# Kernel tuning notes

Hardware: AMD Instinct MI355X
Metric: run time of the kernel (lower is better)

Reference implementation:

```python
import jax, jax.numpy as jnp
import numpy as np

B, S, D = 1024, 48, 256   # graphs, nodes-per-graph, embedding dim (= input_dim)
GDIM = 512                # graph_dim
N = B * S                 # total nodes
E = 4 * N                 # directed edges (avg degree ~4, molecular graphs)
W_SCALE = 0.05


def setup_inputs() -> dict:
    key = jax.random.key(0)
    ks = jax.random.split(key, 8)
    return {
        "sub2gene_out": jax.random.normal(ks[0], (B, S, D), jnp.float32),
        "edge_index": jax.random.randint(ks[1], (2, E), 0, N, dtype=jnp.int64),
        # conv1: in_channels = 2*D (concat of x and laplacian-smoothed x)
        "W_l1": jax.random.normal(ks[2], (GDIM, 2 * D), jnp.float32) * W_SCALE,
        "W_r1": jax.random.normal(ks[3], (GDIM, 2 * D), jnp.float32) * W_SCALE,
        "b1": jnp.zeros((GDIM,), jnp.float32),
        # conv2: graph_dim -> graph_dim
        "W_l2": jax.random.normal(ks[4], (GDIM, GDIM), jnp.float32) * W_SCALE,
        "W_r2": jax.random.normal(ks[5], (GDIM, GDIM), jnp.float32) * W_SCALE,
        "b2": jnp.zeros((GDIM,), jnp.float32),
    }


def sage_conv(x, src, dst, W_l, W_r, b, n):
    """PyG SAGEConv (mean aggregation, root_weight=True):
    out_i = W_l @ mean_{j in N(i)} x_j + W_r @ x_i + b, messages flow src->dst."""
    msg = x[src]                                            # [E, F] gather
    agg = jax.ops.segment_sum(msg, dst, num_segments=n)     # [N, F]
    cnt = jax.ops.segment_sum(jnp.ones((src.shape[0],), x.dtype), dst, num_segments=n)
    mean = agg / jnp.maximum(cnt, 1.0)[:, None]
    return mean @ W_l.T + x @ W_r.T + b


def reference(sub2gene_out, edge_index, W_l1, W_r1, b1, W_l2, W_r2, b2):
    b_, s_, d_ = sub2gene_out.shape
    n = b_ * s_
    x = sub2gene_out.reshape(n, d_)                         # cat of per-graph node features
    row, col = edge_index[0], edge_index[1]

    # sym-normalized Laplacian L = I - D^{-1/2} A D^{-1/2}; lap_x = L @ x
    ones_e = jnp.ones((row.shape[0],), x.dtype)
    deg = jax.ops.segment_sum(ones_e, row, num_segments=n)
    dinv = jnp.where(deg > 0, 1.0, 0.0) / jnp.sqrt(jnp.maximum(deg, 1.0))
    w = -(dinv[row] * dinv[col])                            # off-diagonal -A_norm
    lap_x = x + jax.ops.segment_sum(w[:, None] * x[col], row, num_segments=n)

    x_comb = jnp.concatenate([x, lap_x], axis=-1)           # [N, 2D]
    h = jax.nn.gelu(sage_conv(x_comb, row, col, W_l1, W_r1, b1, n), approximate=False)
    h = sage_conv(h, row, col, W_l2, W_r2, b2, n)           # [N, GDIM]

    # global_mean_pool: every graph has exactly s_ nodes
    batch = jnp.repeat(jnp.arange(b_), s_)
    pooled = jax.ops.segment_sum(h, batch, num_segments=b_) / jnp.asarray(s_, h.dtype)
    return pooled                                           # [B, GDIM]
```

## Files before the change

kernel.cpp:

```cpp
#include <hip/hip_runtime.h>
#include <math.h>

typedef unsigned short u16;
typedef __attribute__((ext_vector_type(8))) short bf16x8;
typedef __attribute__((ext_vector_type(4))) float f32x4;

#define NB 1024
#define NS 48
#define ND 256
#define NN (NB*NS)
#define NE (4*NN)
#define GD 512

__device__ __forceinline__ void gld16(const void* g, void* l) {
  __builtin_amdgcn_global_load_lds(
      (const __attribute__((address_space(1))) void*)(void*)g,
      (__attribute__((address_space(3))) void*)l, 16, 0, 0);
}

__device__ __forceinline__ float bf2f(u16 h) {
  unsigned u = ((unsigned)h) << 16; float f; __builtin_memcpy(&f, &u, 4); return f;
}
__device__ __forceinline__ u16 f2bf(float f) {
  unsigned u; __builtin_memcpy(&u, &f, 4);
  u += 0x7fffu + ((u >> 16) & 1u);
  return (u16)(u >> 16);
}
__device__ __forceinline__ void unpack4(uint2 v, float* f) {
  f[0]=bf2f((u16)(v.x & 0xffff)); f[1]=bf2f((u16)(v.x >> 16));
  f[2]=bf2f((u16)(v.y & 0xffff)); f[3]=bf2f((u16)(v.y >> 16));
}
__device__ __forceinline__ void unpack8(uint4 v, float* f) {
  f[0]=bf2f((u16)(v.x & 0xffff)); f[1]=bf2f((u16)(v.x >> 16));
  f[2]=bf2f((u16)(v.y & 0xffff)); f[3]=bf2f((u16)(v.y >> 16));
  f[4]=bf2f((u16)(v.z & 0xffff)); f[5]=bf2f((u16)(v.z >> 16));
  f[6]=bf2f((u16)(v.w & 0xffff)); f[7]=bf2f((u16)(v.w >> 16));
}
__device__ __forceinline__ uint4 pack8(const float* f) {
  uint4 v;
  v.x = (unsigned)f2bf(f[0]) | ((unsigned)f2bf(f[1]) << 16);
  v.y = (unsigned)f2bf(f[2]) | ((unsigned)f2bf(f[3]) << 16);
  v.z = (unsigned)f2bf(f[4]) | ((unsigned)f2bf(f[5]) << 16);
  v.w = (unsigned)f2bf(f[6]) | ((unsigned)f2bf(f[7]) << 16);
  return v;
}


__global__ void k_hist(const int* __restrict__ ei, int* __restrict__ deg, int* __restrict__ cnt) {
  int e = blockIdx.x * 256 + threadIdx.x;
  if (e < NE) {
    atomicAdd(&deg[ei[e]], 1);
    atomicAdd(&cnt[ei[NE + e]], 1);
  }
}

__global__ void k_dinv(const int* __restrict__ deg, float* __restrict__ dinv) {
  int i = blockIdx.x * 256 + threadIdx.x;
  if (i < NN) dinv[i] = (deg[i] > 0) ? rsqrtf((float)deg[i]) : 0.0f;
}

__global__ void k_exscan(const int* __restrict__ in, int* __restrict__ out) {
  __shared__ int sums[1024];
  const int t = threadIdx.x;
  const int base = t * 48;
  int s = 0;
  for (int i = 0; i < 48; ++i) s += in[base + i];
  sums[t] = s;
  __syncthreads();
  for (int off = 1; off < 1024; off <<= 1) {
    int v = (t >= off) ? sums[t - off] : 0;
    __syncthreads();
    sums[t] += v;
    __syncthreads();
  }
  int run = (t == 0) ? 0 : sums[t - 1];
  for (int i = 0; i < 48; ++i) { int v = in[base + i]; out[base + i] = run; run += v; }
  if (t == 1023) out[NN] = run;
}

__global__ void k_fill(const int* __restrict__ ei,
                       const int* __restrict__ rowOff, const int* __restrict__ colOff,
                       int* __restrict__ rowFill, int* __restrict__ colFill,
                       int* __restrict__ rowCol, int* __restrict__ colSrc) {
  int e = blockIdx.x * 256 + threadIdx.x;
  if (e < NE) {
    int r = ei[e], c = ei[NE + e];
    int pr = atomicAdd(&rowFill[r], 1);
    rowCol[rowOff[r] + pr] = c;
    int pc = atomicAdd(&colFill[c], 1);
    colSrc[colOff[c] + pc] = r;
  }
}

__global__ void k_wcat(const float* __restrict__ W, u16* __restrict__ Wc) {
  int i = (blockIdx.x * 256 + threadIdx.x) * 4;
  float4 v = *(const float4*)(W + i);
  ushort4 h; h.x = f2bf(v.x); h.y = f2bf(v.y); h.z = f2bf(v.z); h.w = f2bf(v.w);
  *(ushort4*)(Wc + i) = h;
}

__global__ void k_x2bf(const float* __restrict__ x, u16* __restrict__ xb) {
  int i = (blockIdx.x * 256 + threadIdx.x) * 8;
  float4 v0 = *(const float4*)(x + i);
  float4 v1 = *(const float4*)(x + i + 4);
  float f[8] = {v0.x, v0.y, v0.z, v0.w, v1.x, v1.y, v1.z, v1.w};
  *(uint4*)(xb + i) = pack8(f);
}

__global__ void k_lap(const u16* __restrict__ xb, const int* __restrict__ rowOff,
                      const int* __restrict__ rowCol, const float* __restrict__ dinv,
                      u16* __restrict__ xc) {
  const int gid = blockIdx.x * 256 + threadIdx.x;
  const int node = gid >> 6, lane = gid & 63;
  float xi[4]; unpack4(*(const uint2*)(xb + (size_t)node * ND + lane * 4), xi);
  float a0 = 0.f, a1 = 0.f, a2 = 0.f, a3 = 0.f;
  const int s0 = rowOff[node], s1 = rowOff[node + 1];
  for (int p = s0; p < s1; p += 4) {
    const int q1 = (p + 1 < s1) ? p + 1 : s1 - 1;
    const int q2 = (p + 2 < s1) ? p + 2 : s1 - 1;
    const int q3 = (p + 3 < s1) ? p + 3 : s1 - 1;
    const int c0 = rowCol[p], c1 = rowCol[q1], c2 = rowCol[q2], c3 = rowCol[q3];
    const float w0 = dinv[c0];
    const float w1 = (p + 1 < s1) ? dinv[c1] : 0.f;
    const float w2 = (p + 2 < s1) ? dinv[c2] : 0.f;
    const float w3 = (p + 3 < s1) ? dinv[c3] : 0.f;
    float f0[4], f1[4], f2[4], f3[4];
    unpack4(*(const uint2*)(xb + (size_t)c0 * ND + lane * 4), f0);
    unpack4(*(const uint2*)(xb + (size_t)c1 * ND + lane * 4), f1);
    unpack4(*(const uint2*)(xb + (size_t)c2 * ND + lane * 4), f2);
    unpack4(*(const uint2*)(xb + (size_t)c3 * ND + lane * 4), f3);
    a0 += w0 * f0[0] + w1 * f1[0] + w2 * f2[0] + w3 * f3[0];
    a1 += w0 * f0[1] + w1 * f1[1] + w2 * f2[1] + w3 * f3[1];
    a2 += w0 * f0[2] + w1 * f1[2] + w2 * f2[2] + w3 * f3[2];
    a3 += w0 * f0[3] + w1 * f1[3] + w2 * f2[3] + w3 * f3[3];
  }
  const float di = dinv[node];
  u16* dst = xc + (size_t)node * GD + lane * 4;
  ushort4 hx; hx.x = f2bf(xi[0]); hx.y = f2bf(xi[1]); hx.z = f2bf(xi[2]); hx.w = f2bf(xi[3]);
  *(ushort4*)dst = hx;
  ushort4 hl; hl.x = f2bf(xi[0] - di * a0); hl.y = f2bf(xi[1] - di * a1);
  hl.z = f2bf(xi[2] - di * a2); hl.w = f2bf(xi[3] - di * a3);
  *(ushort4*)(dst + ND) = hl;
}

__global__ void k_aggx(const u16* __restrict__ xc, const int* __restrict__ colOff,
                       const int* __restrict__ colSrc, u16* __restrict__ xagg) {
  const int gid = blockIdx.x * 256 + threadIdx.x;
  const int node = gid >> 6, lane = gid & 63;
  const int f0 = lane * 8;
  float acc[8] = {};
  const int s0 = colOff[node], s1 = colOff[node + 1];
  for (int p = s0; p < s1; p += 4) {
    const int q1 = (p + 1 < s1) ? p + 1 : s1 - 1;
    const int q2 = (p + 2 < s1) ? p + 2 : s1 - 1;
    const int q3 = (p + 3 < s1) ? p + 3 : s1 - 1;
    const int c0 = colSrc[p], c1 = colSrc[q1], c2 = colSrc[q2], c3 = colSrc[q3];
    const float w1 = (p + 1 < s1) ? 1.f : 0.f;
    const float w2 = (p + 2 < s1) ? 1.f : 0.f;
    const float w3 = (p + 3 < s1) ? 1.f : 0.f;
    float g0[8], g1[8], g2[8], g3[8];
    unpack8(*(const uint4*)(xc + (size_t)c0 * GD + f0), g0);
    unpack8(*(const uint4*)(xc + (size_t)c1 * GD + f0), g1);
    unpack8(*(const uint4*)(xc + (size_t)c2 * GD + f0), g2);
    unpack8(*(const uint4*)(xc + (size_t)c3 * GD + f0), g3);
    #pragma unroll
    for (int j = 0; j < 8; ++j) acc[j] += g0[j] + w1 * g1[j] + w2 * g2[j] + w3 * g3[j];
  }
  const float inv = (s1 > s0) ? 1.0f / (float)(s1 - s0) : 1.0f;
  float res[8];
  #pragma unroll
  for (int j = 0; j < 8; ++j) res[j] = acc[j] * inv;
  *(uint4*)(xagg + (size_t)node * GD + f0) = pack8(res);
}

template <int MODE>
__global__ __launch_bounds__(256) void k_gemm(const u16* __restrict__ A0,
                                              const u16* __restrict__ A1,
                                              const u16* __restrict__ B0,
                                              const u16* __restrict__ B1,
                                              const float* __restrict__ bias,
                                              void* __restrict__ OutP) {
  __shared__ u16 As[128 * 32];
  __shared__ u16 Bs[128 * 32];
  const int tid = threadIdx.x;
  const int w = tid >> 6, lane = tid & 63;
  const int wr = w >> 1, wc = w & 1;

  const int cpx = gridDim.x >> 3;
  const int o = blockIdx.x;
  const int swz = (o & 7) * cpx + (o >> 3);
  const int bx = swz >> 2;
  const int by = swz & 3;

  const int c0 = w * 2, c1 = c0 + 1;
  const int lrow = lane >> 2;
  const int lcol = ((lane & 3) ^ ((lane >> 3) & 3)) * 8;
  const size_t a0r = (size_t)(bx * 128 + c0 * 16 + lrow) * GD + lcol;
  const size_t a1r = (size_t)(bx * 128 + c1 * 16 + lrow) * GD + lcol;
  const size_t b0r = (size_t)(by * 128 + c0 * 16 + lrow) * GD + lcol;
  const size_t b1r = (size_t)(by * 128 + c1 * 16 + lrow) * GD + lcol;
  u16* As0 = As + c0 * 512; u16* As1 = As + c1 * 512;
  u16* Bs0 = Bs + c0 * 512; u16* Bs1 = Bs + c1 * 512;

  const int kslot = ((lane >> 4) ^ ((lane >> 1) & 3)) * 8;
  const int aoff = (wr * 64 + (lane & 15)) * 32 + kslot;
  const int boff = (wc * 64 + (lane & 15)) * 32 + kslot;

  f32x4 acc[4][4] = {};

  for (int kt = 0; kt < 1024; kt += 32) {
    const u16* Asrc = (kt < 512) ? A0 + kt : A1 + (kt - 512);
    const u16* Bsrc = (kt < 512) ? B0 + kt : B1 + (kt - 512);
    gld16(Asrc + a0r, As0);
    gld16(Asrc + a1r, As1);
    gld16(Bsrc + b0r, Bs0);
    gld16(Bsrc + b1r, Bs1);
    __syncthreads();
    bf16x8 aF[4], bF[4];
    #pragma unroll
    for (int i = 0; i < 4; ++i) aF[i] = *(const bf16x8*)(As + aoff + i * 512);
    #pragma unroll
    for (int i = 0; i < 4; ++i) bF[i] = *(const bf16x8*)(Bs + boff + i * 512);
    #pragma unroll
    for (int mi = 0; mi < 4; ++mi)
      #pragma unroll
      for (int ni = 0; ni < 4; ++ni)
        acc[mi][ni] = __builtin_amdgcn_mfma_f32_16x16x32_bf16(aF[mi], bF[ni], acc[mi][ni], 0, 0, 0);
    __syncthreads();
  }

  const int lc = lane & 15, lr = (lane >> 4) * 4;
  const size_t r0 = (size_t)bx * 128 + wr * 64;
  const int cb = by * 128 + wc * 64;
  float bv[4];
  #pragma unroll
  for (int ni = 0; ni < 4; ++ni) bv[ni] = bias[cb + ni * 16 + lc];
  #pragma unroll
  for (int mi = 0; mi < 4; ++mi)
    #pragma unroll
    for (int ni = 0; ni < 4; ++ni)
      #pragma unroll
      for (int r = 0; r < 4; ++r) {
        float v = acc[mi][ni][r] + bv[ni];
        const size_t idx = (r0 + mi * 16 + lr + r) * GD + (cb + ni * 16 + lc);
        if (MODE == 0) {
          v = 0.5f * v * (1.0f + erff(v * 0.70710678118654752f));
          ((u16*)OutP)[idx] = f2bf(v);
        } else {
          ((float*)OutP)[idx] = v;
        }
      }
}

__global__ __launch_bounds__(256) void k_aggh(const u16* __restrict__ h, const int* __restrict__ colOff,
                                              const int* __restrict__ colSrc,
                                              u16* __restrict__ hrb, u16* __restrict__ hab) {
  __shared__ float red[2][4][GD];
  const int g = blockIdx.x;
  const int t = threadIdx.x, w = t >> 6, lane = t & 63;
  const int f0 = lane * 8;
  float pr[8] = {}, pa[8] = {};
  for (int n = w; n < NS; n += 4) {
    const int node = g * NS + n;
    float tmp[8];
    unpack8(*(const uint4*)(h + (size_t)node * GD + f0), tmp);
    #pragma unroll
    for (int j = 0; j < 8; ++j) pr[j] += tmp[j];
    float acc[8] = {};
    const int s0 = colOff[node], s1 = colOff[node + 1];
    for (int p = s0; p < s1; p += 4) {
      const int q1 = (p + 1 < s1) ? p + 1 : s1 - 1;
      const int q2 = (p + 2 < s1) ? p + 2 : s1 - 1;
      const int q3 = (p + 3 < s1) ? p + 3 : s1 - 1;
      const int c0 = colSrc[p], c1 = colSrc[q1], c2 = colSrc[q2], c3 = colSrc[q3];
      const float w1 = (p + 1 < s1) ? 1.f : 0.f;
      const float w2 = (p + 2 < s1) ? 1.f : 0.f;
      const float w3 = (p + 3 < s1) ? 1.f : 0.f;
      float g0[8], g1[8], g2[8], g3[8];
      unpack8(*(const uint4*)(h + (size_t)c0 * GD + f0), g0);
      unpack8(*(const uint4*)(h + (size_t)c1 * GD + f0), g1);
      unpack8(*(const uint4*)(h + (size_t)c2 * GD + f0), g2);
      unpack8(*(const uint4*)(h + (size_t)c3 * GD + f0), g3);
      #pragma unroll
      for (int j = 0; j < 8; ++j) acc[j] += g0[j] + w1 * g1[j] + w2 * g2[j] + w3 * g3[j];
    }
    const float inv = (s1 > s0) ? 1.0f / (float)(s1 - s0) : 1.0f;
    #pragma unroll
    for (int j = 0; j < 8; ++j) pa[j] += acc[j] * inv;
  }
  #pragma unroll
  for (int j = 0; j < 8; ++j) { red[0][w][f0 + j] = pr[j]; red[1][w][f0 + j] = pa[j]; }
  __syncthreads();
  const int f = t * 2;
  const float invS = 1.0f / (float)NS;
  float r0 = (red[0][0][f] + red[0][1][f] + red[0][2][f] + red[0][3][f]) * invS;
  float r1 = (red[0][0][f+1] + red[0][1][f+1] + red[0][2][f+1] + red[0][3][f+1]) * invS;
  float a0 = (red[1][0][f] + red[1][1][f] + red[1][2][f] + red[1][3][f]) * invS;
  float a1 = (red[1][0][f+1] + red[1][1][f+1] + red[1][2][f+1] + red[1][3][f+1]) * invS;
  *(unsigned*)(hrb + (size_t)g * GD + f) = (unsigned)f2bf(r0) | ((unsigned)f2bf(r1) << 16);
  *(unsigned*)(hab + (size_t)g * GD + f) = (unsigned)f2bf(a0) | ((unsigned)f2bf(a1) << 16);
}

extern "C" void kernel_launch(void* const* d_in, const int* in_sizes, int n_in,
                              void* d_out, int out_size, void* d_ws, size_t ws_size,
                              hipStream_t stream) {
  const float* x   = (const float*)d_in[0];
  const int*   ei  = (const int*)d_in[1];
  const float* Wl1 = (const float*)d_in[2];
  const float* Wr1 = (const float*)d_in[3];
  const float* b1  = (const float*)d_in[4];
  const float* Wl2 = (const float*)d_in[5];
  const float* Wr2 = (const float*)d_in[6];
  const float* b2  = (const float*)d_in[7];
  float* out = (float*)d_out;
  (void)in_sizes; (void)n_in; (void)out_size; (void)ws_size;

  int* deg     = (int*)d_ws;
  int* cnt     = deg + NN;
  int* rowFill = cnt + NN;
  int* colFill = rowFill + NN;
  int* rowOff  = colFill + NN;
  int* colOff  = rowOff + NN + 64;
  float* dinv  = (float*)(colOff + NN + 64);
  int* rowCol  = (int*)(dinv + NN);
  int* colSrc  = rowCol + NE;
  u16* WcR1    = (u16*)(colSrc + NE);
  u16* WcL1    = WcR1 + 512 * 512;
  u16* WcR2    = WcL1 + 512 * 512;
  u16* WcL2    = WcR2 + 512 * 512;
  u16* xc      = WcL2 + 512 * 512;
  u16* xagg    = xc + (size_t)NN * GD;
  u16* h       = xagg + (size_t)NN * GD;
  u16* xb      = h;
  u16* hrb     = xagg;
  u16* hab     = xagg + 1024 * GD;

  hipMemsetAsync(deg, 0, sizeof(int) * 4 * NN, stream);

  k_hist<<<NE / 256, 256, 0, stream>>>(ei, deg, cnt);
  k_dinv<<<NN / 256, 256, 0, stream>>>(deg, dinv);
  k_exscan<<<1, 1024, 0, stream>>>(deg, rowOff);
  k_exscan<<<1, 1024, 0, stream>>>(cnt, colOff);
  k_fill<<<NE / 256, 256, 0, stream>>>(ei, rowOff, colOff, rowFill, colFill, rowCol, colSrc);
  k_wcat<<<256, 256, 0, stream>>>(Wr1, WcR1);
  k_wcat<<<256, 256, 0, stream>>>(Wl1, WcL1);
  k_wcat<<<256, 256, 0, stream>>>(Wr2, WcR2);
  k_wcat<<<256, 256, 0, stream>>>(Wl2, WcL2);
  k_x2bf<<<(NN * ND) / (256 * 8), 256, 0, stream>>>(x, xb);
  k_lap<<<(NN * 64) / 256, 256, 0, stream>>>(xb, rowOff, rowCol, dinv, xc);
  k_aggx<<<(NN * 64) / 256, 256, 0, stream>>>(xc, colOff, colSrc, xagg);

  k_gemm<0><<<(NN / 128) * 4, 256, 0, stream>>>(xc, xagg, WcR1, WcL1, b1, (void*)h);

  k_aggh<<<NB, 256, 0, stream>>>(h, colOff, colSrc, hrb, hab);

  k_gemm<1><<<(NB / 128) * 4, 256, 0, stream>>>(hrb, hab, WcR2, WcL2, b2, (void*)out);
}
```

Measured before the change: 295.1 us.

## Double-buffer GEMM LDS tiles and merge scan and weight-convert launches

The bf16 MFMA GEMM now uses two LDS buffers, issuing the next k-tile's global-to-LDS loads before computing the current one, with an explicit vmcnt wait and raw barriers in place of the load-sync-compute-sync loop. The two exclusive-scan launches are merged into one two-block launch, and the four weight-conversion launches into one. The aim is to hide global load latency inside the GEMM and cut kernel launch overhead, at the cost of doubled LDS use per block, which may lower occupancy.

After: 281.3 us. 4.7% less time.

```diff
diff --git a/kernel.cpp b/kernel.cpp
--- a/kernel.cpp
+++ b/kernel.cpp
@@ -59,8 +59,11 @@
   if (i < NN) dinv[i] = (deg[i] > 0) ? rsqrtf((float)deg[i]) : 0.0f;
 }
 
-__global__ void k_exscan(const int* __restrict__ in, int* __restrict__ out) {
+__global__ void k_exscan2(const int* __restrict__ deg, const int* __restrict__ cnt,
+                          int* __restrict__ rowOff, int* __restrict__ colOff) {
   __shared__ int sums[1024];
+  const int* in = blockIdx.x ? cnt : deg;
+  int* out = blockIdx.x ? colOff : rowOff;
   const int t = threadIdx.x;
   const int base = t * 48;
   int s = 0;
@@ -92,9 +95,14 @@
   }
 }
 
-__global__ void k_wcat(const float* __restrict__ W, u16* __restrict__ Wc) {
+__global__ void k_wall(const float* __restrict__ Wr1, const float* __restrict__ Wl1,
+                       const float* __restrict__ Wr2, const float* __restrict__ Wl2,
+                       u16* __restrict__ Wc) {
   int i = (blockIdx.x * 256 + threadIdx.x) * 4;
-  float4 v = *(const float4*)(W + i);
+  int which = i >> 18;
+  int off = i & 262143;
+  const float* W = (which == 0) ? Wr1 : (which == 1) ? Wl1 : (which == 2) ? Wr2 : Wl2;
+  float4 v = *(const float4*)(W + off);
   ushort4 h; h.x = f2bf(v.x); h.y = f2bf(v.y); h.z = f2bf(v.z); h.w = f2bf(v.w);
   *(ushort4*)(Wc + i) = h;
 }
@@ -180,8 +188,8 @@
                                               const u16* __restrict__ B1,
                                               const float* __restrict__ bias,
                                               void* __restrict__ OutP) {
-  __shared__ u16 As[128 * 32];
-  __shared__ u16 Bs[128 * 32];
+  __shared__ u16 As[2][128 * 32];
+  __shared__ u16 Bs[2][128 * 32];
   const int tid = threadIdx.x;
   const int w = tid >> 6, lane = tid & 63;
   const int wr = w >> 1, wc = w & 1;
@@ -199,8 +207,6 @@
   const size_t a1r = (size_t)(bx * 128 + c1 * 16 + lrow) * GD + lcol;
   const size_t b0r = (size_t)(by * 128 + c0 * 16 + lrow) * GD + lcol;
   const size_t b1r = (size_t)(by * 128 + c1 * 16 + lrow) * GD + lcol;
-  u16* As0 = As + c0 * 512; u16* As1 = As + c1 * 512;
-  u16* Bs0 = Bs + c0 * 512; u16* Bs1 = Bs + c1 * 512;
 
   const int kslot = ((lane >> 4) ^ ((lane >> 1) & 3)) * 8;
   const int aoff = (wr * 64 + (lane & 15)) * 32 + kslot;
@@ -208,26 +214,43 @@
 
   f32x4 acc[4][4] = {};
 
-  for (int kt = 0; kt < 1024; kt += 32) {
-    const u16* Asrc = (kt < 512) ? A0 + kt : A1 + (kt - 512);
-    const u16* Bsrc = (kt < 512) ? B0 + kt : B1 + (kt - 512);
-    gld16(Asrc + a0r, As0);
-    gld16(Asrc + a1r, As1);
-    gld16(Bsrc + b0r, Bs0);
-    gld16(Bsrc + b1r, Bs1);
-    __syncthreads();
-    bf16x8 aF[4], bF[4];
-    #pragma unroll
-    for (int i = 0; i < 4; ++i) aF[i] = *(const bf16x8*)(As + aoff + i * 512);
-    #pragma unroll
-    for (int i = 0; i < 4; ++i) bF[i] = *(const bf16x8*)(Bs + boff + i * 512);
-    #pragma unroll
-    for (int mi = 0; mi < 4; ++mi)
-      #pragma unroll
-      for (int ni = 0; ni < 4; ++ni)
-        acc[mi][ni] = __builtin_amdgcn_mfma_f32_16x16x32_bf16(aF[mi], bF[ni], acc[mi][ni], 0, 0, 0);
-    __syncthreads();
-  }
+  #define STAGE(kt, buf) do {                                              \
+    const u16* Asrc_ = ((kt) < 512) ? A0 + (kt) : A1 + ((kt) - 512);       \
+    const u16* Bsrc_ = ((kt) < 512) ? B0 + (kt) : B1 + ((kt) - 512);       \
+    gld16(Asrc_ + a0r, As[buf] + c0 * 512);                                \
+    gld16(Asrc_ + a1r, As[buf] + c1 * 512);                                \
+    gld16(Bsrc_ + b0r, Bs[buf] + c0 * 512);                                \
+    gld16(Bsrc_ + b1r, Bs[buf] + c1 * 512);                                \
+  } while (0)
+
+  #define COMPUTE(buf) do {                                                \
+    bf16x8 aF[4], bF[4];                                                   \
+    _Pragma("unroll")                                                      \
+    for (int i = 0; i < 4; ++i) aF[i] = *(const bf16x8*)(As[buf] + aoff + i * 512); \
+    _Pragma("unroll")                                                      \
+    for (int i = 0; i < 4; ++i) bF[i] = *(const bf16x8*)(Bs[buf] + boff + i * 512); \
+    _Pragma("unroll")                                                      \
+    for (int mi = 0; mi < 4; ++mi)                                         \
+      _Pragma("unroll")                                                    \
+      for (int ni = 0; ni < 4; ++ni)                                       \
+        acc[mi][ni] = __builtin_amdgcn_mfma_f32_16x16x32_bf16(aF[mi], bF[ni], acc[mi][ni], 0, 0, 0); \
+  } while (0)
+
+  STAGE(0, 0);
+  int cur = 0;
+  for (int t = 0; t < 31; ++t) {
+    STAGE((t + 1) * 32, cur ^ 1);
+    asm volatile("s_waitcnt vmcnt(4)" ::: "memory");
+    __builtin_amdgcn_s_barrier();
+    COMPUTE(cur);
+    __builtin_amdgcn_s_barrier();
+    cur ^= 1;
+  }
+  asm volatile("s_waitcnt vmcnt(0)" ::: "memory");
+  __builtin_amdgcn_s_barrier();
+  COMPUTE(cur);
+  #undef STAGE
+  #undef COMPUTE
 
   const int lc = lane & 15, lr = (lane >> 4) * 4;
   const size_t r0 = (size_t)bx * 128 + wr * 64;
@@ -339,13 +362,9 @@
 
   k_hist<<<NE / 256, 256, 0, stream>>>(ei, deg, cnt);
   k_dinv<<<NN / 256, 256, 0, stream>>>(deg, dinv);
-  k_exscan<<<1, 1024, 0, stream>>>(deg, rowOff);
-  k_exscan<<<1, 1024, 0, stream>>>(cnt, colOff);
+  k_exscan2<<<2, 1024, 0, stream>>>(deg, cnt, rowOff, colOff);
   k_fill<<<NE / 256, 256, 0, stream>>>(ei, rowOff, colOff, rowFill, colFill, rowCol, colSrc);
-  k_wcat<<<256, 256, 0, stream>>>(Wr1, WcR1);
-  k_wcat<<<256, 256, 0, stream>>>(Wl1, WcL1);
-  k_wcat<<<256, 256, 0, stream>>>(Wr2, WcR2);
-  k_wcat<<<256, 256, 0, stream>>>(Wl2, WcL2);
+  k_wall<<<1024, 256, 0, stream>>>(Wr1, Wl1, Wr2, Wl2, WcR1);
   k_x2bf<<<(NN * ND) / (256 * 8), 256, 0, stream>>>(x, xb);
   k_lap<<<(NN * 64) / 256, 256, 0, stream>>>(xb, rowOff, rowCol, dinv, xc);
   k_aggx<<<(NN * 64) / 256, 256, 0, stream>>>(xc, colOff, colSrc, xagg);
```

## Merge small setup kernels, widen Laplacian gather, split GEMM K loop

Applied to the files above, without the earlier changes.

Folds the dinv computation and both exclusive scans into one three-block launch. Merges the four weight conversions and the x-to-bf16 conversion into one kernel. The Laplacian kernel now handles two nodes per wavefront with 8-element (16-byte) loads, halving its grid. The GEMM K loop is split into two unrolled halves so the per-iteration source-pointer selects go away. Together these cut launch count and per-thread overhead, at the cost of a few branches inside the fused kernels.

New measurement: 288.2 us. 1.02x faster.

```diff
diff --git a/kernel.cpp b/kernel.cpp
--- a/kernel.cpp
+++ b/kernel.cpp
@@ -25,10 +25,6 @@
   unsigned u; __builtin_memcpy(&u, &f, 4);
   u += 0x7fffu + ((u >> 16) & 1u);
   return (u16)(u >> 16);
-}
-__device__ __forceinline__ void unpack4(uint2 v, float* f) {
-  f[0]=bf2f((u16)(v.x & 0xffff)); f[1]=bf2f((u16)(v.x >> 16));
-  f[2]=bf2f((u16)(v.y & 0xffff)); f[3]=bf2f((u16)(v.y >> 16));
 }
 __device__ __forceinline__ void unpack8(uint4 v, float* f) {
   f[0]=bf2f((u16)(v.x & 0xffff)); f[1]=bf2f((u16)(v.x >> 16));
@@ -54,15 +50,21 @@
   }
 }
 
-__global__ void k_dinv(const int* __restrict__ deg, float* __restrict__ dinv) {
-  int i = blockIdx.x * 256 + threadIdx.x;
-  if (i < NN) dinv[i] = (deg[i] > 0) ? rsqrtf((float)deg[i]) : 0.0f;
-}
-
-__global__ void k_exscan(const int* __restrict__ in, int* __restrict__ out) {
-  __shared__ int sums[1024];
+__global__ void k_exscan2(const int* __restrict__ deg, const int* __restrict__ cnt,
+                          int* __restrict__ rowOff, int* __restrict__ colOff,
+                          float* __restrict__ dinv) {
   const int t = threadIdx.x;
   const int base = t * 48;
+  if (blockIdx.x == 2) {
+    for (int i = 0; i < 48; ++i) {
+      int d = deg[base + i];
+      dinv[base + i] = (d > 0) ? rsqrtf((float)d) : 0.0f;
+    }
+    return;
+  }
+  __shared__ int sums[1024];
+  const int* in = blockIdx.x ? cnt : deg;
+  int* out = blockIdx.x ? colOff : rowOff;
   int s = 0;
   for (int i = 0; i < 48; ++i) s += in[base + i];
   sums[t] = s;
@@ -92,28 +94,35 @@
   }
 }
 
-__global__ void k_wcat(const float* __restrict__ W, u16* __restrict__ Wc) {
-  int i = (blockIdx.x * 256 + threadIdx.x) * 4;
-  float4 v = *(const float4*)(W + i);
-  ushort4 h; h.x = f2bf(v.x); h.y = f2bf(v.y); h.z = f2bf(v.z); h.w = f2bf(v.w);
-  *(ushort4*)(Wc + i) = h;
-}
-
-__global__ void k_x2bf(const float* __restrict__ x, u16* __restrict__ xb) {
-  int i = (blockIdx.x * 256 + threadIdx.x) * 8;
-  float4 v0 = *(const float4*)(x + i);
-  float4 v1 = *(const float4*)(x + i + 4);
-  float f[8] = {v0.x, v0.y, v0.z, v0.w, v1.x, v1.y, v1.z, v1.w};
-  *(uint4*)(xb + i) = pack8(f);
+__global__ void k_wx(const float* __restrict__ Wr1, const float* __restrict__ Wl1,
+                     const float* __restrict__ Wr2, const float* __restrict__ Wl2,
+                     u16* __restrict__ Wc, const float* __restrict__ x, u16* __restrict__ xb) {
+  if (blockIdx.x < 1024) {
+    int i = (blockIdx.x * 256 + threadIdx.x) * 4;
+    int which = i >> 18;
+    int off = i & 262143;
+    const float* W = (which == 0) ? Wr1 : (which == 1) ? Wl1 : (which == 2) ? Wr2 : Wl2;
+    float4 v = *(const float4*)(W + off);
+    ushort4 h; h.x = f2bf(v.x); h.y = f2bf(v.y); h.z = f2bf(v.z); h.w = f2bf(v.w);
+    *(ushort4*)(Wc + i) = h;
+  } else {
+    int i = ((blockIdx.x - 1024) * 256 + threadIdx.x) * 8;
+    float4 v0 = *(const float4*)(x + i);
+    float4 v1 = *(const float4*)(x + i + 4);
+    float f[8] = {v0.x, v0.y, v0.z, v0.w, v1.x, v1.y, v1.z, v1.w};
+    *(uint4*)(xb + i) = pack8(f);
+  }
 }
 
 __global__ void k_lap(const u16* __restrict__ xb, const int* __restrict__ rowOff,
                       const int* __restrict__ rowCol, const float* __restrict__ dinv,
                       u16* __restrict__ xc) {
   const int gid = blockIdx.x * 256 + threadIdx.x;
-  const int node = gid >> 6, lane = gid & 63;
-  float xi[4]; unpack4(*(const uint2*)(xb + (size_t)node * ND + lane * 4), xi);
-  float a0 = 0.f, a1 = 0.f, a2 = 0.f, a3 = 0.f;
+  const int wid = gid >> 6, lane = gid & 63;
+  const int node = wid * 2 + (lane >> 5);
+  const int f0 = (lane & 31) * 8;
+  float xi[8]; unpack8(*(const uint4*)(xb + (size_t)node * ND + f0), xi);
+  float a[8] = {};
   const int s0 = rowOff[node], s1 = rowOff[node + 1];
   for (int p = s0; p < s1; p += 4) {
     const int q1 = (p + 1 < s1) ? p + 1 : s1 - 1;
@@ -124,23 +133,21 @@
     const float w1 = (p + 1 < s1) ? dinv[c1] : 0.f;
     const float w2 = (p + 2 < s1) ? dinv[c2] : 0.f;
     const float w3 = (p + 3 < s1) ? dinv[c3] : 0.f;
-    float f0[4], f1[4], f2[4], f3[4];
-    unpack4(*(const uint2*)(xb + (size_t)c0 * ND + lane * 4), f0);
-    unpack4(*(const uint2*)(xb + (size_t)c1 * ND + lane * 4), f1);
-    unpack4(*(const uint2*)(xb + (size_t)c2 * ND + lane * 4), f2);
-    unpack4(*(const uint2*)(xb + (size_t)c3 * ND + lane * 4), f3);
-    a0 += w0 * f0[0] + w1 * f1[0] + w2 * f2[0] + w3 * f3[0];
-    a1 += w0 * f0[1] + w1 * f1[1] + w2 * f2[1] + w3 * f3[1];
-    a2 += w0 * f0[2] + w1 * f1[2] + w2 * f2[2] + w3 * f3[2];
-    a3 += w0 * f0[3] + w1 * f1[3] + w2 * f2[3] + w3 * f3[3];
+    float g0[8], g1[8], g2[8], g3[8];
+    unpack8(*(const uint4*)(xb + (size_t)c0 * ND + f0), g0);
+    unpack8(*(const uint4*)(xb + (size_t)c1 * ND + f0), g1);
+    unpack8(*(const uint4*)(xb + (size_t)c2 * ND + f0), g2);
+    unpack8(*(const uint4*)(xb + (size_t)c3 * ND + f0), g3);
+    #pragma unroll
+    for (int j = 0; j < 8; ++j) a[j] += w0 * g0[j] + w1 * g1[j] + w2 * g2[j] + w3 * g3[j];
   }
   const float di = dinv[node];
-  u16* dst = xc + (size_t)node * GD + lane * 4;
-  ushort4 hx; hx.x = f2bf(xi[0]); hx.y = f2bf(xi[1]); hx.z = f2bf(xi[2]); hx.w = f2bf(xi[3]);
-  *(ushort4*)dst = hx;
-  ushort4 hl; hl.x = f2bf(xi[0] - di * a0); hl.y = f2bf(xi[1] - di * a1);
-  hl.z = f2bf(xi[2] - di * a2); hl.w = f2bf(xi[3] - di * a3);
-  *(ushort4*)(dst + ND) = hl;
+  u16* dst = xc + (size_t)node * GD + f0;
+  *(uint4*)dst = pack8(xi);
+  float l[8];
+  #pragma unroll
+  for (int j = 0; j < 8; ++j) l[j] = xi[j] - di * a[j];
+  *(uint4*)(dst + ND) = pack8(l);
 }
 
 __global__ void k_aggx(const u16* __restrict__ xc, const int* __restrict__ colOff,
@@ -208,25 +215,28 @@
 
   f32x4 acc[4][4] = {};
 
-  for (int kt = 0; kt < 1024; kt += 32) {
-    const u16* Asrc = (kt < 512) ? A0 + kt : A1 + (kt - 512);
-    const u16* Bsrc = (kt < 512) ? B0 + kt : B1 + (kt - 512);
-    gld16(Asrc + a0r, As0);
-    gld16(Asrc + a1r, As1);
-    gld16(Bsrc + b0r, Bs0);
-    gld16(Bsrc + b1r, Bs1);
-    __syncthreads();
-    bf16x8 aF[4], bF[4];
-    #pragma unroll
-    for (int i = 0; i < 4; ++i) aF[i] = *(const bf16x8*)(As + aoff + i * 512);
-    #pragma unroll
-    for (int i = 0; i < 4; ++i) bF[i] = *(const bf16x8*)(Bs + boff + i * 512);
-    #pragma unroll
-    for (int mi = 0; mi < 4; ++mi)
-      #pragma unroll
-      for (int ni = 0; ni < 4; ++ni)
-        acc[mi][ni] = __builtin_amdgcn_mfma_f32_16x16x32_bf16(aF[mi], bF[ni], acc[mi][ni], 0, 0, 0);
-    __syncthreads();
+  #pragma unroll
+  for (int half = 0; half < 2; ++half) {
+    const u16* Ab = half ? A1 : A0;
+    const u16* Bb = half ? B1 : B0;
+    for (int kt = 0; kt < 512; kt += 32) {
+      gld16(Ab + kt + a0r, As0);
+      gld16(Ab + kt + a1r, As1);
+      gld16(Bb + kt + b0r, Bs0);
+      gld16(Bb + kt + b1r, Bs1);
+      __syncthreads();
+      bf16x8 aF[4], bF[4];
+      #pragma unroll
+      for (int i = 0; i < 4; ++i) aF[i] = *(const bf16x8*)(As + aoff + i * 512);
+      #pragma unroll
+      for (int i = 0; i < 4; ++i) bF[i] = *(const bf16x8*)(Bs + boff + i * 512);
+      #pragma unroll
+      for (int mi = 0; mi < 4; ++mi)
+        #pragma unroll
+        for (int ni = 0; ni < 4; ++ni)
+          acc[mi][ni] = __builtin_amdgcn_mfma_f32_16x16x32_bf16(aF[mi], bF[ni], acc[mi][ni], 0, 0, 0);
+      __syncthreads();
+    }
   }
 
   const int lc = lane & 15, lr = (lane >> 4) * 4;
@@ -338,16 +348,10 @@
   hipMemsetAsync(deg, 0, sizeof(int) * 4 * NN, stream);
 
   k_hist<<<NE / 256, 256, 0, stream>>>(ei, deg, cnt);
-  k_dinv<<<NN / 256, 256, 0, stream>>>(deg, dinv);
-  k_exscan<<<1, 1024, 0, stream>>>(deg, rowOff);
-  k_exscan<<<1, 1024, 0, stream>>>(cnt, colOff);
+  k_exscan2<<<3, 1024, 0, stream>>>(deg, cnt, rowOff, colOff, dinv);
   k_fill<<<NE / 256, 256, 0, stream>>>(ei, rowOff, colOff, rowFill, colFill, rowCol, colSrc);
-  k_wcat<<<256, 256, 0, stream>>>(Wr1, WcR1);
-  k_wcat<<<256, 256, 0, stream>>>(Wl1, WcL1);
-  k_wcat<<<256, 256, 0, stream>>>(Wr2, WcR2);
-  k_wcat<<<256, 256, 0, stream>>>(Wl2, WcL2);
-  k_x2bf<<<(NN * ND) / (256 * 8), 256, 0, stream>>>(x, xb);
-  k_lap<<<(NN * 64) / 256, 256, 0, stream>>>(xb, rowOff, rowCol, dinv, xc);
+  k_wx<<<1024 + (NN * ND) / (256 * 8), 256, 0, stream>>>(Wr1, Wl1, Wr2, Wl2, WcR1, x, xb);
+  k_lap<<<(NN * 32) / 256, 256, 0, stream>>>(xb, rowOff, rowCol, dinv, xc);
   k_aggx<<<(NN * 64) / 256, 256, 0, stream>>>(xc, colOff, colSrc, xagg);
 
   k_gemm<0><<<(NN / 128) * 4, 256, 0, stream>>>(xc, xagg, WcR1, WcL1, b1, (void*)h);
```
